# Performance work log

Hardware: AMD Instinct MI355X
Metric: run time of the kernel (lower is better)

The kernel has to match this reference:

```python
import jax, jax.numpy as jnp
import numpy as np

D_MODEL = 1024
NUM_HEADS = 16
D_K = D_MODEL // NUM_HEADS
BATCH = 4
SEQ = 2048


def setup_inputs() -> dict:
    key = jax.random.key(0)
    ks = jax.random.split(key, 12)
    s = 0.02
    inp = {
        "Q": jax.random.normal(ks[0], (BATCH, SEQ, D_MODEL), jnp.float32),
        "K": jax.random.normal(ks[1], (BATCH, SEQ, D_MODEL), jnp.float32),
        "V": jax.random.normal(ks[2], (BATCH, SEQ, D_MODEL), jnp.float32),
        "mask": jnp.tril(jnp.ones((SEQ, SEQ), jnp.int32)),  # causal: 0 = masked
        "Wq": jax.random.normal(ks[3], (D_MODEL, D_MODEL), jnp.float32) * s,
        "bq": jax.random.normal(ks[4], (D_MODEL,), jnp.float32) * s,
        "Wk": jax.random.normal(ks[5], (D_MODEL, D_MODEL), jnp.float32) * s,
        "bk": jax.random.normal(ks[6], (D_MODEL,), jnp.float32) * s,
        "Wv": jax.random.normal(ks[7], (D_MODEL, D_MODEL), jnp.float32) * s,
        "bv": jax.random.normal(ks[8], (D_MODEL,), jnp.float32) * s,
        "Wo": jax.random.normal(ks[9], (D_MODEL, D_MODEL), jnp.float32) * s,
        "bo": jax.random.normal(ks[10], (D_MODEL,), jnp.float32) * s,
    }
    return inp


def _split_heads(x):
    # (b, s, d_model) -> (b, h, s, d_k)
    b, s, _ = x.shape
    return x.reshape(b, s, NUM_HEADS, D_K).transpose(0, 2, 1, 3)


def reference(Q, K, V, mask, Wq, bq, Wk, bk, Wv, bv, Wo, bo):
    # Linear projections (torch Linear: x @ W^T + b)
    q = _split_heads(Q @ Wq.T + bq)  # (b, h, s, dk)
    k = _split_heads(K @ Wk.T + bk)
    v = _split_heads(V @ Wv.T + bv)
    scale = 1.0 / jnp.sqrt(jnp.asarray(D_K, q.dtype))
    scores = jnp.einsum("bhqd,bhkd->bhqk", q, k) * scale  # (b, h, s, s)
    scores = jnp.where(mask == 0, jnp.asarray(-jnp.inf, scores.dtype), scores)
    attn = jax.nn.softmax(scores, axis=-1)
    out = jnp.einsum("bhqk,bhkd->bhqd", attn, v)  # (b, h, s, dk)
    b, h, s, dk = out.shape
    out = out.transpose(0, 2, 1, 3).reshape(b, s, h * dk)  # combine heads
    return out @ Wo.T + bo
```

## Files before the change

### kernel.cpp

```cpp
#include <hip/hip_runtime.h>


typedef _Float16 f16;
typedef _Float16 f16x8 __attribute__((ext_vector_type(8)));
typedef _Float16 f16x4 __attribute__((ext_vector_type(4)));
typedef float floatx4 __attribute__((ext_vector_type(4)));

#define SEQ 2048
#define DM 1024
#define NH 16
#define DK 64
#define MR 8192

__device__ __forceinline__ void gl_lds16(const void* g, void* lds) {
    __builtin_amdgcn_global_load_lds(
        (const __attribute__((address_space(1))) unsigned int*)g,
        (__attribute__((address_space(3))) unsigned int*)lds,
        16, 0, 0);
}

struct ConvArgs {
    const float* s[7];
    f16* d[7];
};

__global__ __launch_bounds__(256) void convk(ConvArgs a) {
    int bx = blockIdx.x;
    int t, base;
    if (bx < 3 * 8192) { t = bx / 8192; base = bx - t * 8192; }
    else { int r = bx - 3 * 8192; t = 3 + r / 1024; base = r - (t - 3) * 1024; }
    int i = base * 256 + threadIdx.x;
    float4 v = ((const float4*)a.s[t])[i];
    f16x4 o;
    o.x = (f16)v.x; o.y = (f16)v.y; o.z = (f16)v.z; o.w = (f16)v.w;
    ((f16x4*)a.d[t])[i] = o;
}

template <int MODE>
__device__ __forceinline__ void gemm_body(
    const f16* __restrict__ A, const f16* __restrict__ W,
    const float* __restrict__ bias, void* __restrict__ outp,
    int m0, int n0, f16* As, f16* Bs)
{
    const int tid = threadIdx.x;
    const int wave = tid >> 6, lane = tid & 63;
    const int quad = lane >> 4, ln = lane & 15;
    const int wr = wave >> 1, wc = wave & 1;

    floatx4 acc[4][4] = {};

    for (int kt = 0; kt < 16; ++kt) {
        const int k0 = kt * 64;
#pragma unroll
        for (int s = 0; s < 4; ++s) {
            int c = s * 256 + tid;
            int row = c >> 3, lc = (c & 7) ^ (row & 7);
            gl_lds16(A + (size_t)(m0 + row) * 1024 + k0 + lc * 8,
                     (char*)As + (s * 256 + wave * 64) * 16);
        }
#pragma unroll
        for (int s = 0; s < 4; ++s) {
            int c = s * 256 + tid;
            int row = c >> 3, lc = (c & 7) ^ (row & 7);
            gl_lds16(W + (size_t)(n0 + row) * 1024 + k0 + lc * 8,
                     (char*)Bs + (s * 256 + wave * 64) * 16);
        }
        __syncthreads();
#pragma unroll
        for (int kk = 0; kk < 64; kk += 32) {
            const int cb = kk >> 3;
            f16x8 af[4], bf[4];
#pragma unroll
            for (int i = 0; i < 4; ++i) {
                int row = wr * 64 + i * 16 + ln;
                af[i] = *(const f16x8*)&As[row * 64 + (((cb + quad) ^ (ln & 7)) << 3)];
            }
#pragma unroll
            for (int j = 0; j < 4; ++j) {
                int row = wc * 64 + j * 16 + ln;
                bf[j] = *(const f16x8*)&Bs[row * 64 + (((cb + quad) ^ (ln & 7)) << 3)];
            }
#pragma unroll
            for (int i = 0; i < 4; ++i)
#pragma unroll
                for (int j = 0; j < 4; ++j)
                    acc[i][j] = __builtin_amdgcn_mfma_f32_16x16x32_f16(
                        af[i], bf[j], acc[i][j], 0, 0, 0);
        }
        __syncthreads();
    }

#pragma unroll
    for (int i = 0; i < 4; ++i) {
#pragma unroll
        for (int j = 0; j < 4; ++j) {
            int col = n0 + wc * 64 + j * 16 + ln;
            float bc = bias[col];
            int rowb = m0 + wr * 64 + i * 16 + quad * 4;
#pragma unroll
            for (int r = 0; r < 4; ++r) {
                float v = acc[i][j][r] + bc;
                int rm = rowb + r;
                if (MODE == 2) {
                    ((float*)outp)[(size_t)rm * 1024 + col] = v;
                } else {
                    int bb = rm >> 11, ss = rm & 2047;
                    int hh = col >> 6, dd = col & 63;
                    f16* o = (f16*)outp;
                    if (MODE == 0)
                        o[(((size_t)(bb * 16 + hh)) * 2048 + ss) * 64 + dd] = (f16)v;
                    else
                        o[(((size_t)(bb * 16 + hh)) * 64 + dd) * 2048 + ss] = (f16)v;
                }
            }
        }
    }
}

struct G3Args {
    const f16* A[3]; const f16* W[3]; const float* b[3]; f16* o[3];
};

__global__ __launch_bounds__(256, 2) void gemm_qkv(G3Args g) {
    __shared__ alignas(16) f16 As[128 * 64];
    __shared__ alignas(16) f16 Bs[128 * 64];
    const int z = blockIdx.z;
    const int m0 = blockIdx.x * 128, n0 = blockIdx.y * 128;
    if (z < 2)
        gemm_body<0>(g.A[z], g.W[z], g.b[z], g.o[z], m0, n0, As, Bs);
    else
        gemm_body<1>(g.A[2], g.W[2], g.b[2], g.o[2], m0, n0, As, Bs);
}

__global__ __launch_bounds__(256, 2) void gemm_out(
    const f16* __restrict__ A, const f16* __restrict__ W,
    const float* __restrict__ bias, float* __restrict__ outp)
{
    __shared__ alignas(16) f16 As[128 * 64];
    __shared__ alignas(16) f16 Bs[128 * 64];
    gemm_body<2>(A, W, bias, outp, blockIdx.x * 128, blockIdx.y * 128, As, Bs);
}

__global__ __launch_bounds__(256, 2) void attn_kernel(
    const f16* __restrict__ Qp, const f16* __restrict__ Kp,
    const f16* __restrict__ Vt, f16* __restrict__ Op)
{
    __shared__ alignas(16) f16 ks[128 * 64];
    __shared__ alignas(16) f16 vs[64 * 128];
    __shared__ alignas(16) f16 ps[128 * 128];

    const int tid = threadIdx.x;
    const int wave = tid >> 6, lane = tid & 63;
    const int quad = lane >> 4, ln = lane & 15;
    const int bh = blockIdx.x;
    const f16* qb = Qp + (size_t)bh * SEQ * DK;
    const f16* kb = Kp + (size_t)bh * SEQ * DK;
    const f16* vb = Vt + (size_t)bh * DK * SEQ;
    const int b = bh >> 4, h = bh & 15;

    f16* pslot = ps + wave * 4096;

    f16x8 ones;
#pragma unroll
    for (int e = 0; e < 8; ++e) ones[e] = (f16)1.0f;

    for (int half = 0; half < 2; ++half) {
        const int jt = half ? (15 - blockIdx.y) : blockIdx.y;
        const int q0 = jt * 128;

#pragma unroll
        for (int s = 0; s < 4; ++s) {
            int c = s * 256 + tid;
            int row = c >> 3, lc = (c & 7) ^ (row & 7);
            gl_lds16(qb + (size_t)(q0 + row) * 64 + lc * 8,
                     (char*)ps + (s * 256 + wave * 64) * 16);
        }
        __syncthreads();
        f16x8 aq[2][2];
#pragma unroll
        for (int mt = 0; mt < 2; ++mt)
#pragma unroll
            for (int kk = 0; kk < 2; ++kk) {
                int row = wave * 32 + mt * 16 + ln;
                f16x8 v = *(const f16x8*)&ps[row * 64 + (((kk * 4 + quad) ^ (ln & 7)) << 3)];
#pragma unroll
                for (int e = 0; e < 8; ++e) v[e] = v[e] * (f16)0.125f;
                aq[mt][kk] = v;
            }

        floatx4 oacc[2][4] = {};
        floatx4 lacc[2] = {};

        const int nk = jt + 1;
        for (int kt = 0; kt < nk; ++kt) {
            const int k0 = kt * 128;
#pragma unroll
            for (int s = 0; s < 4; ++s) {
                int c = s * 256 + tid;
                int row = c >> 3, lc = (c & 7) ^ (row & 7);
                gl_lds16(kb + (size_t)(k0 + row) * 64 + lc * 8,
                         (char*)ks + (s * 256 + wave * 64) * 16);
            }
#pragma unroll
            for (int s = 0; s < 4; ++s) {
                int c = s * 256 + tid;
                int row = c >> 4, lc = (c & 15) ^ (row & 15);
                gl_lds16(vb + (size_t)row * SEQ + k0 + lc * 8,
                         (char*)vs + (s * 256 + wave * 64) * 16);
            }
            __syncthreads();

            floatx4 sacc[2][8] = {};
#pragma unroll
            for (int kk = 0; kk < 2; ++kk) {
                const int pc = ((kk * 4 + quad) ^ (ln & 7)) << 3;
#pragma unroll
                for (int nt = 0; nt < 8; ++nt) {
                    f16x8 bk = *(const f16x8*)&ks[(nt * 16 + ln) * 64 + pc];
#pragma unroll
                    for (int mt = 0; mt < 2; ++mt)
                        sacc[mt][nt] = __builtin_amdgcn_mfma_f32_16x16x32_f16(
                            aq[mt][kk], bk, sacc[mt][nt], 0, 0, 0);
                }
            }

            const bool diag = (k0 == q0);
#pragma unroll
            for (int mt = 0; mt < 2; ++mt) {
                const int rowb = q0 + wave * 32 + mt * 16 + quad * 4;
#pragma unroll
                for (int nt = 0; nt < 8; ++nt) {
                    const int lch = nt * 2 + (ln >> 3);
                    const int off = ln & 7;
                    const int colv = k0 + nt * 16 + ln;
#pragma unroll
                    for (int r = 0; r < 4; ++r) {
                        float t = sacc[mt][nt][r];
                        if (diag && colv > rowb + r) t = -1e30f;
                        float p = __expf(t);
                        int rp = mt * 16 + quad * 4 + r;
                        pslot[rp * 128 + ((lch ^ (rp & 15)) << 3) + off] = (f16)p;
                    }
                }
            }

#pragma unroll
            for (int kk4 = 0; kk4 < 4; ++kk4) {
                f16x8 ap[2];
#pragma unroll
                for (int mt = 0; mt < 2; ++mt) {
                    int rp = mt * 16 + ln;
                    ap[mt] = *(const f16x8*)&pslot[rp * 128 + (((kk4 * 4 + quad) ^ ln) << 3)];
                    lacc[mt] = __builtin_amdgcn_mfma_f32_16x16x32_f16(
                        ap[mt], ones, lacc[mt], 0, 0, 0);
                }
#pragma unroll
                for (int nt2 = 0; nt2 < 4; ++nt2) {
                    int row = nt2 * 16 + ln;
                    f16x8 bv = *(const f16x8*)&vs[row * 128 + (((kk4 * 4 + quad) ^ ln) << 3)];
#pragma unroll
                    for (int mt = 0; mt < 2; ++mt)
                        oacc[mt][nt2] = __builtin_amdgcn_mfma_f32_16x16x32_f16(
                            ap[mt], bv, oacc[mt][nt2], 0, 0, 0);
                }
            }
            __syncthreads();
        }

#pragma unroll
        for (int mt = 0; mt < 2; ++mt) {
            int rowb = q0 + wave * 32 + mt * 16 + quad * 4;
            float inv[4];
#pragma unroll
            for (int r = 0; r < 4; ++r) inv[r] = 1.0f / lacc[mt][r];
#pragma unroll
            for (int nt2 = 0; nt2 < 4; ++nt2) {
                int col = h * 64 + nt2 * 16 + ln;
#pragma unroll
                for (int r = 0; r < 4; ++r) {
                    float v = oacc[mt][nt2][r] * inv[r];
                    Op[((size_t)b * SEQ + rowb + r) * DM + col] = (f16)v;
                }
            }
        }
    }
}

extern "C" void kernel_launch(void* const* d_in, const int* in_sizes, int n_in,
                              void* d_out, int out_size, void* d_ws, size_t ws_size,
                              hipStream_t stream) {
    const float* Q  = (const float*)d_in[0];
    const float* K  = (const float*)d_in[1];
    const float* V  = (const float*)d_in[2];
    const float* Wq = (const float*)d_in[4];
    const float* bq = (const float*)d_in[5];
    const float* Wk = (const float*)d_in[6];
    const float* bk = (const float*)d_in[7];
    const float* Wv = (const float*)d_in[8];
    const float* bv = (const float*)d_in[9];
    const float* Wo = (const float*)d_in[10];
    const float* bo = (const float*)d_in[11];

    char* ws = (char*)d_ws;
    f16* Xq  = (f16*)(ws);
    f16* Xk  = Xq + (size_t)MR * DM;
    f16* Xv  = Xk + (size_t)MR * DM;
    f16* Wqb = Xv + (size_t)MR * DM;
    f16* Wkb = Wqb + (size_t)DM * DM;
    f16* Wvb = Wkb + (size_t)DM * DM;
    f16* Wob = Wvb + (size_t)DM * DM;
    f16* qp  = Wob + (size_t)DM * DM;
    f16* kp  = qp + (size_t)MR * DM;
    f16* vtp = kp + (size_t)MR * DM;

    ConvArgs ca;
    ca.s[0] = Q;  ca.d[0] = Xq;
    ca.s[1] = K;  ca.d[1] = Xk;
    ca.s[2] = V;  ca.d[2] = Xv;
    ca.s[3] = Wq; ca.d[3] = Wqb;
    ca.s[4] = Wk; ca.d[4] = Wkb;
    ca.s[5] = Wv; ca.d[5] = Wvb;
    ca.s[6] = Wo; ca.d[6] = Wob;
    convk<<<3 * 8192 + 4 * 1024, 256, 0, stream>>>(ca);

    G3Args g;
    g.A[0] = Xq; g.W[0] = Wqb; g.b[0] = bq; g.o[0] = qp;
    g.A[1] = Xk; g.W[1] = Wkb; g.b[1] = bk; g.o[1] = kp;
    g.A[2] = Xv; g.W[2] = Wvb; g.b[2] = bv; g.o[2] = vtp;
    gemm_qkv<<<dim3(64, 8, 3), 256, 0, stream>>>(g);

    attn_kernel<<<dim3(64, 8), 256, 0, stream>>>(qp, kp, vtp, Xq);

    gemm_out<<<dim3(64, 8), 256, 0, stream>>>(Xq, Wob, bo, (float*)d_out);
}
```

Measured before the change: 308.6 us.

## Specialize diagonal attention tile, use exp2 with folded log2e, retune occupancy

The attention inner loop moves into a templated helper, so off-diagonal tiles skip the causal-mask compare and only the final diagonal tile applies it. The Q prescale now folds log2(e) into the 1/sqrt(dk) factor so the raw exp2 intrinsic can replace __expf. The P-tile LDS swizzle gains an extra XOR term to change the bank mapping between writes and reads. Separately, both GEMM kernels' launch bounds rise from 2 to 4 waves per SIMD, which may force register spilling in exchange for higher occupancy.

```diff
diff --git a/kernel.cpp b/kernel.cpp
--- a/kernel.cpp
+++ b/kernel.cpp
@@ -121,7 +121,7 @@
     const f16* A[3]; const f16* W[3]; const float* b[3]; f16* o[3];
 };
 
-__global__ __launch_bounds__(256, 2) void gemm_qkv(G3Args g) {
+__global__ __launch_bounds__(256, 4) void gemm_qkv(G3Args g) {
     __shared__ alignas(16) f16 As[128 * 64];
     __shared__ alignas(16) f16 Bs[128 * 64];
     const int z = blockIdx.z;
@@ -132,13 +132,95 @@
         gemm_body<1>(g.A[2], g.W[2], g.b[2], g.o[2], m0, n0, As, Bs);
 }
 
-__global__ __launch_bounds__(256, 2) void gemm_out(
+__global__ __launch_bounds__(256, 4) void gemm_out(
     const f16* __restrict__ A, const f16* __restrict__ W,
     const float* __restrict__ bias, float* __restrict__ outp)
 {
     __shared__ alignas(16) f16 As[128 * 64];
     __shared__ alignas(16) f16 Bs[128 * 64];
     gemm_body<2>(A, W, bias, outp, blockIdx.x * 128, blockIdx.y * 128, As, Bs);
+}
+
+template <bool DIAG>
+__device__ __forceinline__ void attn_iter(
+    const f16* kb, const f16* vb, int k0, int q0,
+    f16* ks, f16* vs, f16* pslot,
+    int tid, int wave, int quad, int ln,
+    const f16x8 (&aq)[2][2], const f16x8& ones,
+    floatx4 (&oacc)[2][4], floatx4 (&lacc)[2])
+{
+#pragma unroll
+    for (int s = 0; s < 4; ++s) {
+        int c = s * 256 + tid;
+        int row = c >> 3, lc = (c & 7) ^ (row & 7);
+        gl_lds16(kb + (size_t)(k0 + row) * 64 + lc * 8,
+                 (char*)ks + (s * 256 + wave * 64) * 16);
+    }
+#pragma unroll
+    for (int s = 0; s < 4; ++s) {
+        int c = s * 256 + tid;
+        int row = c >> 4, lc = (c & 15) ^ (row & 15);
+        gl_lds16(vb + (size_t)row * SEQ + k0 + lc * 8,
+                 (char*)vs + (s * 256 + wave * 64) * 16);
+    }
+    __syncthreads();
+
+    floatx4 sacc[2][8] = {};
+#pragma unroll
+    for (int kk = 0; kk < 2; ++kk) {
+        const int pc = ((kk * 4 + quad) ^ (ln & 7)) << 3;
+#pragma unroll
+        for (int nt = 0; nt < 8; ++nt) {
+            f16x8 bk = *(const f16x8*)&ks[(nt * 16 + ln) * 64 + pc];
+#pragma unroll
+            for (int mt = 0; mt < 2; ++mt)
+                sacc[mt][nt] = __builtin_amdgcn_mfma_f32_16x16x32_f16(
+                    aq[mt][kk], bk, sacc[mt][nt], 0, 0, 0);
+        }
+    }
+
+#pragma unroll
+    for (int mt = 0; mt < 2; ++mt) {
+        const int rowb = q0 + wave * 32 + mt * 16 + quad * 4;
+#pragma unroll
+        for (int nt = 0; nt < 8; ++nt) {
+            const int lch = nt * 2 + (ln >> 3);
+            const int off = ln & 7;
+            const int colv = k0 + nt * 16 + ln;
+#pragma unroll
+            for (int r = 0; r < 4; ++r) {
+                float t = sacc[mt][nt][r];
+                if (DIAG && colv > rowb + r) t = -1e30f;
+                float p = __builtin_amdgcn_exp2f(t);
+                const int rp = mt * 16 + quad * 4 + r;
+                const int sw = (rp & 15) ^ (((rp >> 3) & 1) << 1);
+                pslot[rp * 128 + ((lch ^ sw) << 3) + off] = (f16)p;
+            }
+        }
+    }
+
+#pragma unroll
+    for (int kk4 = 0; kk4 < 4; ++kk4) {
+        f16x8 ap[2];
+#pragma unroll
+        for (int mt = 0; mt < 2; ++mt) {
+            const int rp = mt * 16 + ln;
+            const int sw = (rp & 15) ^ (((rp >> 3) & 1) << 1);
+            ap[mt] = *(const f16x8*)&pslot[rp * 128 + (((kk4 * 4 + quad) ^ sw) << 3)];
+            lacc[mt] = __builtin_amdgcn_mfma_f32_16x16x32_f16(
+                ap[mt], ones, lacc[mt], 0, 0, 0);
+        }
+#pragma unroll
+        for (int nt2 = 0; nt2 < 4; ++nt2) {
+            int row = nt2 * 16 + ln;
+            f16x8 bv = *(const f16x8*)&vs[row * 128 + (((kk4 * 4 + quad) ^ ln) << 3)];
+#pragma unroll
+            for (int mt = 0; mt < 2; ++mt)
+                oacc[mt][nt2] = __builtin_amdgcn_mfma_f32_16x16x32_f16(
+                    ap[mt], bv, oacc[mt][nt2], 0, 0, 0);
+        }
+    }
+    __syncthreads();
 }
 
 __global__ __launch_bounds__(256, 2) void attn_kernel(
@@ -184,7 +266,8 @@
                 int row = wave * 32 + mt * 16 + ln;
                 f16x8 v = *(const f16x8*)&ps[row * 64 + (((kk * 4 + quad) ^ (ln & 7)) << 3)];
 #pragma unroll
-                for (int e = 0; e < 8; ++e) v[e] = v[e] * (f16)0.125f;
+                for (int e = 0; e < 8; ++e)
+                    v[e] = v[e] * (f16)0.18033688f;
                 aq[mt][kk] = v;
             }
 
@@ -192,80 +275,11 @@
         floatx4 lacc[2] = {};
 
         const int nk = jt + 1;
-        for (int kt = 0; kt < nk; ++kt) {
-            const int k0 = kt * 128;
-#pragma unroll
-            for (int s = 0; s < 4; ++s) {
-                int c = s * 256 + tid;
-                int row = c >> 3, lc = (c & 7) ^ (row & 7);
-                gl_lds16(kb + (size_t)(k0 + row) * 64 + lc * 8,
-                         (char*)ks + (s * 256 + wave * 64) * 16);
-            }
-#pragma unroll
-            for (int s = 0; s < 4; ++s) {
-                int c = s * 256 + tid;
-                int row = c >> 4, lc = (c & 15) ^ (row & 15);
-                gl_lds16(vb + (size_t)row * SEQ + k0 + lc * 8,
-                         (char*)vs + (s * 256 + wave * 64) * 16);
-            }
-            __syncthreads();
-
-            floatx4 sacc[2][8] = {};
-#pragma unroll
-            for (int kk = 0; kk < 2; ++kk) {
-                const int pc = ((kk * 4 + quad) ^ (ln & 7)) << 3;
-#pragma unroll
-                for (int nt = 0; nt < 8; ++nt) {
-                    f16x8 bk = *(const f16x8*)&ks[(nt * 16 + ln) * 64 + pc];
-#pragma unroll
-                    for (int mt = 0; mt < 2; ++mt)
-                        sacc[mt][nt] = __builtin_amdgcn_mfma_f32_16x16x32_f16(
-                            aq[mt][kk], bk, sacc[mt][nt], 0, 0, 0);
-                }
-            }
-
-            const bool diag = (k0 == q0);
-#pragma unroll
-            for (int mt = 0; mt < 2; ++mt) {
-                const int rowb = q0 + wave * 32 + mt * 16 + quad * 4;
-#pragma unroll
-                for (int nt = 0; nt < 8; ++nt) {
-                    const int lch = nt * 2 + (ln >> 3);
-                    const int off = ln & 7;
-                    const int colv = k0 + nt * 16 + ln;
-#pragma unroll
-                    for (int r = 0; r < 4; ++r) {
-                        float t = sacc[mt][nt][r];
-                        if (diag && colv > rowb + r) t = -1e30f;
-                        float p = __expf(t);
-                        int rp = mt * 16 + quad * 4 + r;
-                        pslot[rp * 128 + ((lch ^ (rp & 15)) << 3) + off] = (f16)p;
-                    }
-                }
-            }
-
-#pragma unroll
-            for (int kk4 = 0; kk4 < 4; ++kk4) {
-                f16x8 ap[2];
-#pragma unroll
-                for (int mt = 0; mt < 2; ++mt) {
-                    int rp = mt * 16 + ln;
-                    ap[mt] = *(const f16x8*)&pslot[rp * 128 + (((kk4 * 4 + quad) ^ ln) << 3)];
-                    lacc[mt] = __builtin_amdgcn_mfma_f32_16x16x32_f16(
-                        ap[mt], ones, lacc[mt], 0, 0, 0);
-                }
-#pragma unroll
-                for (int nt2 = 0; nt2 < 4; ++nt2) {
-                    int row = nt2 * 16 + ln;
-                    f16x8 bv = *(const f16x8*)&vs[row * 128 + (((kk4 * 4 + quad) ^ ln) << 3)];
-#pragma unroll
-                    for (int mt = 0; mt < 2; ++mt)
-                        oacc[mt][nt2] = __builtin_amdgcn_mfma_f32_16x16x32_f16(
-                            ap[mt], bv, oacc[mt][nt2], 0, 0, 0);
-                }
-            }
-            __syncthreads();
-        }
+        for (int kt = 0; kt < nk - 1; ++kt)
+            attn_iter<false>(kb, vb, kt * 128, q0, ks, vs, pslot,
+                             tid, wave, quad, ln, aq, ones, oacc, lacc);
+        attn_iter<true>(kb, vb, (nk - 1) * 128, q0, ks, vs, pslot,
+                        tid, wave, quad, ln, aq, ones, oacc, lacc);
 
 #pragma unroll
         for (int mt = 0; mt < 2; ++mt) {
```

New measurement: 314.3 us. About the same (+1.9%).
